# Kernel optimization log

Hardware: AMD Instinct MI355X
Metric: run time of the kernel (lower is better)

## Reference

```python
import jax, jax.numpy as jnp
import numpy as np

WS = (4, 4, 4)          # window size (d, h, w)
NUM_HEADS = 6
DIM = 192


def _relative_position_index(ws):
    # static int index, computed in numpy
    coords = np.stack(np.meshgrid(np.arange(ws[0]), np.arange(ws[1]), np.arange(ws[2]), indexing='ij'))  # (3, wd, wh, ww)
    coords = coords.reshape(3, -1)                      # (3, N)
    rel = coords[:, :, None] - coords[:, None, :]        # (3, N, N)
    rel = rel.transpose(1, 2, 0)                         # (N, N, 3)
    rel[:, :, 0] += ws[0] - 1
    rel[:, :, 1] += ws[1] - 1
    rel[:, :, 2] += ws[2] - 1
    rel[:, :, 0] *= (2 * ws[1] - 1) * (2 * ws[2] - 1)
    rel[:, :, 1] *= (2 * ws[2] - 1)
    return rel.sum(-1)                                   # (N, N)

_REL_IDX = _relative_position_index(WS)


def setup_inputs() -> dict:
    key = jax.random.key(0)
    ks = jax.random.split(key, 4)
    x = jax.random.normal(ks[0], (2, DIM, 46, 47, 48), dtype=jnp.float32)
    qkv_w = jax.random.normal(ks[1], (3 * DIM, DIM), dtype=jnp.float32) * 0.02
    qkv_b = jnp.zeros((3 * DIM,), dtype=jnp.float32)
    proj_w = jax.random.normal(ks[2], (DIM, DIM), dtype=jnp.float32) * 0.02
    proj_b = jnp.zeros((DIM,), dtype=jnp.float32)
    rpb_table = jax.random.normal(ks[3], ((2 * WS[0] - 1) * (2 * WS[1] - 1) * (2 * WS[2] - 1), NUM_HEADS), dtype=jnp.float32) * 0.02
    return {"x": x, "qkv_w": qkv_w, "qkv_b": qkv_b, "proj_w": proj_w, "proj_b": proj_b, "rpb_table": rpb_table}


def reference(x, qkv_w, qkv_b, proj_w, proj_b, rpb_table):
    B, C, D, H, W = x.shape
    wd, wh, ww = WS
    pd = (-D) % wd
    ph = (-H) % wh
    pw = (-W) % ww
    Dp, Hp, Wp = D + pd, H + ph, W + pw

    # BCDHW -> B,D,H,W,C then pad spatial dims (zero pad, same as F.pad on BCDHW)
    xc = jnp.transpose(x, (0, 2, 3, 4, 1))
    xc = jnp.pad(xc, ((0, 0), (0, pd), (0, ph), (0, pw), (0, 0)))

    # window partition -> (nW, N, C)
    Dw, Hw, Ww = Dp // wd, Hp // wh, Wp // ww
    xw = xc.reshape(B, Dw, wd, Hw, wh, Ww, ww, C)
    xw = jnp.transpose(xw, (0, 1, 3, 5, 2, 4, 6, 7)).reshape(-1, wd * wh * ww, C)
    N = wd * wh * ww

    # windowed MHA with relative position bias
    hd = C // NUM_HEADS
    qkv = xw @ qkv_w.T + qkv_b                               # (nW, N, 3C)
    qkv = qkv.reshape(-1, N, 3, NUM_HEADS, hd)
    q, k, v = (jnp.transpose(qkv[:, :, i], (0, 2, 1, 3)) for i in range(3))  # (nW, h, N, hd)
    scale = jnp.asarray(hd, x.dtype) ** -0.5
    attn = jnp.einsum('whnd,whmd->whnm', q * scale, k)       # (nW, h, N, N)
    bias = rpb_table[_REL_IDX.reshape(-1)].reshape(N, N, NUM_HEADS)
    bias = jnp.transpose(bias, (2, 0, 1))                    # (h, N, N)
    attn = jax.nn.softmax(attn + bias[None], axis=-1)
    out = jnp.einsum('whnm,whmd->whnd', attn, v)             # (nW, h, N, hd)
    out = jnp.transpose(out, (0, 2, 1, 3)).reshape(-1, N, C)
    out = out @ proj_w.T + proj_b

    # window reverse + crop, back to BCDHW
    xr = out.reshape(B, Dw, Hw, Ww, wd, wh, ww, C)
    xr = jnp.transpose(xr, (0, 1, 4, 2, 5, 3, 6, 7)).reshape(B, Dp, Hp, Wp, C)
    xr = jnp.transpose(xr, (0, 4, 1, 2, 3))[:, :, :D, :H, :W]
    return xr
```

## Files before the change

kernel.cpp:

```cpp
#include <hip/hip_runtime.h>

typedef __bf16 bf16x8 __attribute__((ext_vector_type(8)));
typedef __bf16 bf16x4 __attribute__((ext_vector_type(4)));
typedef float  f32x4  __attribute__((ext_vector_type(4)));

#define MFMA16(a, b, c) __builtin_amdgcn_mfma_f32_16x16x32_bf16((a), (b), (c), 0, 0, 0)

constexpr int Cdim = 192, NHd = 6;
constexpr int Dd = 46, Hh = 47, Wl = 48;
constexpr int HWst = Hh * Wl;
constexpr int NWIN_PER_B = 12 * 12 * 12;
constexpr int NBLK = 2 * NWIN_PER_B;
constexpr float SCALE = 0.17677669529663687f;

constexpr int WQ_ELEMS = 576 * 192;
constexpr int WP_ELEMS = 192 * 192;
constexpr size_t OFF_WQ   = 0;
constexpr size_t OFF_WP   = OFF_WQ + WQ_ELEMS;
constexpr size_t OFF_RPBT = OFF_WP + WP_ELEMS;
constexpr size_t WS_SMALL = (OFF_RPBT + 4128) * 2;

__device__ inline bf16x8 cvt8(const float* __restrict__ p) {
  f32x4 u0 = *(const f32x4*)p;
  f32x4 u1 = *(const f32x4*)(p + 4);
  bf16x8 r;
  r[0] = (__bf16)u0[0]; r[1] = (__bf16)u0[1]; r[2] = (__bf16)u0[2]; r[3] = (__bf16)u0[3];
  r[4] = (__bf16)u1[0]; r[5] = (__bf16)u1[1]; r[6] = (__bf16)u1[2]; r[7] = (__bf16)u1[3];
  return r;
}

__device__ inline bf16x8 cat8(bf16x4 a, bf16x4 b) {
  bf16x8 r;
  r[0] = a[0]; r[1] = a[1]; r[2] = a[2]; r[3] = a[3];
  r[4] = b[0]; r[5] = b[1]; r[6] = b[2]; r[7] = b[3];
  return r;
}

__global__ __launch_bounds__(256) void convert_w_kernel(
    const float* __restrict__ qkv_w, const float* __restrict__ proj_w,
    const float* __restrict__ rpb,
    __bf16* __restrict__ wq, __bf16* __restrict__ wp, float* __restrict__ rpbt) {
  const int i = blockIdx.x * 256 + threadIdx.x;
  if (i < WQ_ELEMS) wq[i] = (__bf16)qkv_w[i];
  if (i < WP_ELEMS) wp[i] = (__bf16)proj_w[i];
  if (i < 343 * NHd) {
    const int h = i / 343, idx = i % 343;
    rpbt[h * 343 + idx] = rpb[idx * NHd + h];
  }
}

constexpr int QKLD = 36;
constexpr int VLD  = 68;
constexpr int PLD  = 72;
constexpr int BUFE = 2304;

__global__ __launch_bounds__(384, 4) void fused_kernel(
    const float* __restrict__ x, const float* __restrict__ qkv_b,
    const __bf16* __restrict__ wq, const __bf16* __restrict__ wp,
    const float* __restrict__ proj_b, const float* __restrict__ rpbt,
    float* __restrict__ out)
{
  __shared__ __bf16 xw[64 * 200];
  __shared__ __bf16 bufs[6 * BUFE];
  const f32x4 fz = {0.f, 0.f, 0.f, 0.f};
  const int tid = threadIdx.x, lane = tid & 63, wv = tid >> 6;
  const int li = lane & 15, g = lane >> 4;
  const int hq = wv;
  const int bid = blockIdx.x;
  const int wid = (bid & 7) * (NBLK / 8) + (bid >> 3);
  const int b = wid / NWIN_PER_B, wr = wid % NWIN_PER_B;
  const int d0 = (wr / 144) * 4, h0 = ((wr / 12) % 12) * 4, w0 = (wr % 12) * 4;

  #pragma unroll
  for (int rep = 0; rep < 8; ++rep) {
    const int task = rep * 384 + tid;
    const int c = task % Cdim, ph = task / Cdim;
    const int dd = ph >> 2, hh = ph & 3;
    const int d = d0 + dd, hs = h0 + hh;
    f32x4 v = fz;
    if (d < Dd && hs < Hh)
      v = *(const f32x4*)(x + ((size_t)(b * Cdim + c) * Dd + d) * HWst + hs * Wl + w0);
    const int nb = (dd * 16 + hh * 4) * 200 + c;
    xw[nb]       = (__bf16)v[0];
    xw[nb + 200] = (__bf16)v[1];
    xw[nb + 400] = (__bf16)v[2];
    xw[nb + 600] = (__bf16)v[3];
  }
  __syncthreads();

  __bf16* buf = bufs + wv * BUFE;
  bf16x8 qfv[4], kfv[4], vav[2][2];

  {
    f32x4 acc[2][4];
    #pragma unroll
    for (int i = 0; i < 2; ++i)
      #pragma unroll
      for (int t = 0; t < 4; ++t) acc[i][t] = fz;
    #pragma unroll
    for (int kk = 0; kk < 6; ++kk) {
      const int k0 = kk * 32 + g * 8;
      bf16x8 xf[4];
      #pragma unroll
      for (int nt = 0; nt < 4; ++nt)
        xf[nt] = *(const bf16x8*)&xw[(nt * 16 + li) * 200 + k0];
      #pragma unroll
      for (int i = 0; i < 2; ++i) {
        bf16x8 wf = *(const bf16x8*)(wq + (size_t)((hq * 2 + i) * 16 + li) * Cdim + k0);
        #pragma unroll
        for (int nt = 0; nt < 4; ++nt)
          acc[i][nt] = MFMA16(wf, xf[nt], acc[i][nt]);
      }
    }
    #pragma unroll
    for (int i = 0; i < 2; ++i) {
      const f32x4 b4 = *(const f32x4*)(qkv_b + (hq * 2 + i) * 16 + g * 4);
      #pragma unroll
      for (int nt = 0; nt < 4; ++nt) {
        f32x4 val = (acc[i][nt] + b4) * SCALE;
        bf16x4 pk;
        pk[0] = (__bf16)val[0]; pk[1] = (__bf16)val[1];
        pk[2] = (__bf16)val[2]; pk[3] = (__bf16)val[3];
        *(bf16x4*)&buf[(nt * 16 + li) * QKLD + i * 16 + g * 4] = pk;
      }
    }
    #pragma unroll
    for (int t = 0; t < 4; ++t) {
      bf16x4 lo = *(const bf16x4*)&buf[(t * 16 + li) * QKLD + g * 8];
      bf16x4 hi = *(const bf16x4*)&buf[(t * 16 + li) * QKLD + g * 8 + 4];
      qfv[t] = cat8(lo, hi);
    }
  }

  {
    f32x4 acc[2][4];
    #pragma unroll
    for (int i = 0; i < 2; ++i)
      #pragma unroll
      for (int t = 0; t < 4; ++t) acc[i][t] = fz;
    #pragma unroll
    for (int kk = 0; kk < 6; ++kk) {
      const int k0 = kk * 32 + g * 8;
      bf16x8 xf[4];
      #pragma unroll
      for (int nt = 0; nt < 4; ++nt)
        xf[nt] = *(const bf16x8*)&xw[(nt * 16 + li) * 200 + k0];
      #pragma unroll
      for (int i = 0; i < 2; ++i) {
        bf16x8 wf = *(const bf16x8*)(wq + (size_t)(192 + (hq * 2 + i) * 16 + li) * Cdim + k0);
        #pragma unroll
        for (int nt = 0; nt < 4; ++nt)
          acc[i][nt] = MFMA16(wf, xf[nt], acc[i][nt]);
      }
    }
    #pragma unroll
    for (int i = 0; i < 2; ++i) {
      const f32x4 b4 = *(const f32x4*)(qkv_b + 192 + (hq * 2 + i) * 16 + g * 4);
      #pragma unroll
      for (int nt = 0; nt < 4; ++nt) {
        f32x4 val = acc[i][nt] + b4;
        bf16x4 pk;
        pk[0] = (__bf16)val[0]; pk[1] = (__bf16)val[1];
        pk[2] = (__bf16)val[2]; pk[3] = (__bf16)val[3];
        *(bf16x4*)&buf[(nt * 16 + li) * QKLD + i * 16 + g * 4] = pk;
      }
    }
    #pragma unroll
    for (int t = 0; t < 4; ++t) {
      bf16x4 lo = *(const bf16x4*)&buf[(t * 16 + li) * QKLD + g * 8];
      bf16x4 hi = *(const bf16x4*)&buf[(t * 16 + li) * QKLD + g * 8 + 4];
      kfv[t] = cat8(lo, hi);
    }
  }

  {
    f32x4 acc[2][4];
    #pragma unroll
    for (int i = 0; i < 2; ++i)
      #pragma unroll
      for (int t = 0; t < 4; ++t) acc[i][t] = fz;
    #pragma unroll
    for (int kk = 0; kk < 6; ++kk) {
      const int k0 = kk * 32 + g * 8;
      bf16x8 xf[4];
      #pragma unroll
      for (int rt = 0; rt < 4; ++rt)
        xf[rt] = *(const bf16x8*)&xw[(rt * 16 + li) * 200 + k0];
      #pragma unroll
      for (int i = 0; i < 2; ++i) {
        bf16x8 wf = *(const bf16x8*)(wq + (size_t)(384 + (hq * 2 + i) * 16 + li) * Cdim + k0);
        #pragma unroll
        for (int rt = 0; rt < 4; ++rt)
          acc[i][rt] = MFMA16(xf[rt], wf, acc[i][rt]);
      }
    }
    #pragma unroll
    for (int i = 0; i < 2; ++i) {
      const float bias = qkv_b[384 + (hq * 2 + i) * 16 + li];
      #pragma unroll
      for (int rt = 0; rt < 4; ++rt) {
        bf16x4 pk;
        pk[0] = (__bf16)(acc[i][rt][0] + bias);
        pk[1] = (__bf16)(acc[i][rt][1] + bias);
        pk[2] = (__bf16)(acc[i][rt][2] + bias);
        pk[3] = (__bf16)(acc[i][rt][3] + bias);
        *(bf16x4*)&buf[(i * 16 + li) * VLD + rt * 16 + g * 4] = pk;
      }
    }
    #pragma unroll
    for (int rt = 0; rt < 2; ++rt)
      #pragma unroll
      for (int kk = 0; kk < 2; ++kk) {
        bf16x4 lo = *(const bf16x4*)&buf[(rt * 16 + li) * VLD + kk * 32 + g * 8];
        bf16x4 hi = *(const bf16x4*)&buf[(rt * 16 + li) * VLD + kk * 32 + g * 8 + 4];
        vav[rt][kk] = cat8(lo, hi);
      }
  }
  __syncthreads();

  __bf16* ao = xw;

  const int hbase = ((li >> 2) - g + 3) * 7 + (li & 3) + 3;
  float brow[7][4];
  {
    const float* rp = rpbt + hq * 343 + hbase - 3;
    #pragma unroll
    for (int dd = 0; dd < 7; ++dd)
      #pragma unroll
      for (int j = 0; j < 4; ++j)
        brow[dd][j] = rp[dd * 49 + j];
  }

  __bf16* pw = buf;

  #pragma unroll
  for (int rb = 0; rb < 4; ++rb) {
    f32x4 s[4];
    #pragma unroll
    for (int ct = 0; ct < 4; ++ct) s[ct] = MFMA16(kfv[ct], qfv[rb], fz);

    float t[4][4];
    float rm = -3e38f;
    #pragma unroll
    for (int ct = 0; ct < 4; ++ct) {
      #pragma unroll
      for (int r = 0; r < 4; ++r) {
        const float tv = s[ct][r] + brow[rb - ct + 3][3 - r];
        t[ct][r] = tv;
        rm = fmaxf(rm, tv);
      }
    }
    rm = fmaxf(rm, __shfl_xor(rm, 16));
    rm = fmaxf(rm, __shfl_xor(rm, 32));
    float rs = 0.f;
    #pragma unroll
    for (int ct = 0; ct < 4; ++ct)
      #pragma unroll
      for (int r = 0; r < 4; ++r) {
        const float p = __expf(t[ct][r] - rm);
        t[ct][r] = p;
        rs += p;
      }
    rs += __shfl_xor(rs, 16);
    rs += __shfl_xor(rs, 32);
    const float rinv = 1.f / rs;

    #pragma unroll
    for (int ct = 0; ct < 4; ++ct) {
      bf16x4 pk;
      pk[0] = (__bf16)(t[ct][0] * rinv);
      pk[1] = (__bf16)(t[ct][1] * rinv);
      pk[2] = (__bf16)(t[ct][2] * rinv);
      pk[3] = (__bf16)(t[ct][3] * rinv);
      *(bf16x4*)&pw[li * PLD + ct * 16 + g * 4] = pk;
    }
    bf16x8 pa0 = *(const bf16x8*)&pw[li * PLD + g * 8];
    bf16x8 pa1 = *(const bf16x8*)&pw[li * PLD + 32 + g * 8];
    f32x4 o0 = fz, o1 = fz;
    o0 = MFMA16(vav[0][0], pa0, o0);
    o0 = MFMA16(vav[0][1], pa1, o0);
    o1 = MFMA16(vav[1][0], pa0, o1);
    o1 = MFMA16(vav[1][1], pa1, o1);
    #pragma unroll
    for (int rt = 0; rt < 2; ++rt) {
      const f32x4 o = rt ? o1 : o0;
      bf16x4 pk;
      pk[0] = (__bf16)o[0]; pk[1] = (__bf16)o[1];
      pk[2] = (__bf16)o[2]; pk[3] = (__bf16)o[3];
      *(bf16x4*)&ao[(rb * 16 + li) * 200 + hq * 32 + rt * 16 + g * 4] = pk;
    }
  }
  __syncthreads();

  f32x4 pacc[2][4];
  #pragma unroll
  for (int i = 0; i < 2; ++i)
    #pragma unroll
    for (int rt = 0; rt < 4; ++rt) pacc[i][rt] = fz;
  #pragma unroll
  for (int kk = 0; kk < 6; ++kk) {
    const int k0 = kk * 32 + g * 8;
    bf16x8 af[4];
    #pragma unroll
    for (int rt = 0; rt < 4; ++rt)
      af[rt] = *(const bf16x8*)&ao[(rt * 16 + li) * 200 + k0];
    #pragma unroll
    for (int i = 0; i < 2; ++i) {
      const int c = (wv * 2 + i) * 16 + li;
      bf16x8 bf = *(const bf16x8*)(wp + (size_t)c * Cdim + k0);
      #pragma unroll
      for (int rt = 0; rt < 4; ++rt)
        pacc[i][rt] = MFMA16(af[rt], bf, pacc[i][rt]);
    }
  }
  #pragma unroll
  for (int i = 0; i < 2; ++i) {
    const int c = (wv * 2 + i) * 16 + li;
    const float pb = proj_b[c];
    #pragma unroll
    for (int rt = 0; rt < 4; ++rt) {
      const int d = d0 + rt, hs = h0 + g;
      if (d < Dd && hs < Hh) {
        f32x4 vv = {pacc[i][rt][0] + pb, pacc[i][rt][1] + pb,
                    pacc[i][rt][2] + pb, pacc[i][rt][3] + pb};
        *(f32x4*)(out + ((size_t)(b * Cdim + c) * Dd + d) * HWst + hs * Wl + w0) = vv;
      }
    }
  }
}

constexpr int XW_LD = 200, QK_LD = 36, VT_LD = 68, P_LDF = 68;
constexpr int XW_OFF  = 0;
constexpr int Q_OFF   = 25600;
constexpr int K_OFF   = Q_OFF + 27648;
constexpr int VT_OFF  = K_OFF + 27648;
constexpr int P_OFF   = VT_OFF + 26112;
constexpr int RPB_OFF = P_OFF + 26112;
constexpr int LDS_TOTAL = RPB_OFF + 8256;

__global__ __launch_bounds__(768, 3) void winattn_fused(
    const float* __restrict__ x, const float* __restrict__ qkv_w,
    const float* __restrict__ qkv_b, const float* __restrict__ proj_w,
    const float* __restrict__ proj_b, const float* __restrict__ rpb,
    float* __restrict__ out)
{
  extern __shared__ __align__(16) char smem[];
  __bf16* xw  = (__bf16*)(smem + XW_OFF);
  __bf16* qs  = (__bf16*)(smem + Q_OFF);
  __bf16* ks  = (__bf16*)(smem + K_OFF);
  __bf16* vt  = (__bf16*)(smem + VT_OFF);
  __bf16* pl  = (__bf16*)(smem + P_OFF);
  float*  rps = (float*)(smem + RPB_OFF);
  const f32x4 fz = {0.f, 0.f, 0.f, 0.f};
  const int tid = threadIdx.x, lane = tid & 63, wv = tid >> 6;
  const int hq = wv >> 1, half = wv & 1, li = lane & 15, g = lane >> 4;
  const int bid = blockIdx.x;
  const int wid = (bid & 7) * (NBLK / 8) + (bid >> 3);
  const int b = wid / NWIN_PER_B, wr = wid % NWIN_PER_B;
  const int d0 = (wr / 144) * 4, h0 = ((wr / 12) % 12) * 4, w0 = (wr % 12) * 4;
  for (int i = tid; i < 343 * NHd; i += 768) rps[i] = rpb[i];
  #pragma unroll
  for (int rep = 0; rep < 4; ++rep) {
    const int task = rep * 768 + tid;
    const int c = task % Cdim, ph = task / Cdim;
    const int dd = ph >> 2, hh2 = ph & 3;
    const int d = d0 + dd, hsp = h0 + hh2;
    f32x4 v = fz;
    if (d < Dd && hsp < Hh)
      v = *(const f32x4*)(x + ((size_t)(b * Cdim + c) * Dd + d) * HWst + hsp * Wl + w0);
    const int nb = (dd * 16 + hh2 * 4) * XW_LD + c;
    xw[nb] = (__bf16)v[0]; xw[nb + XW_LD] = (__bf16)v[1];
    xw[nb + 2 * XW_LD] = (__bf16)v[2]; xw[nb + 3 * XW_LD] = (__bf16)v[3];
  }
  __syncthreads();
  {
    f32x4 acc[6][2];
    #pragma unroll
    for (int it = 0; it < 6; ++it)
      #pragma unroll
      for (int rr = 0; rr < 2; ++rr) acc[it][rr] = fz;
    #pragma unroll
    for (int kk = 0; kk < 6; ++kk) {
      const int k0 = kk * 32 + g * 8;
      bf16x8 af[2];
      #pragma unroll
      for (int rr = 0; rr < 2; ++rr)
        af[rr] = *(const bf16x8*)&xw[((half * 2 + rr) * 16 + li) * XW_LD + k0];
      #pragma unroll
      for (int it = 0; it < 6; ++it) {
        const int T = (it >> 1) * 12 + hq * 2 + (it & 1);
        const int j = T * 16 + li;
        bf16x8 bf = cvt8(qkv_w + j * Cdim + k0);
        #pragma unroll
        for (int rr = 0; rr < 2; ++rr) acc[it][rr] = MFMA16(af[rr], bf, acc[it][rr]);
      }
    }
    #pragma unroll
    for (int it = 0; it < 6; ++it) {
      const int part = it >> 1, e16 = (it & 1) * 16;
      const int j0 = (part * 12 + hq * 2 + (it & 1)) * 16;
      const float qb = qkv_b[j0 + li];
      #pragma unroll
      for (int rr = 0; rr < 2; ++rr) {
        const int rb = half * 2 + rr;
        #pragma unroll
        for (int r = 0; r < 4; ++r) {
          const float val = acc[it][rr][r] + qb;
          const int n = rb * 16 + g * 4 + r;
          if (part == 0)      qs[(hq * 64 + n) * QK_LD + e16 + li] = (__bf16)val;
          else if (part == 1) ks[(hq * 64 + n) * QK_LD + e16 + li] = (__bf16)val;
          else                vt[(hq * 32 + e16 + li) * VT_LD + n] = (__bf16)val;
        }
      }
    }
  }
  __syncthreads();
  {
    __bf16* pw = pl + wv * 16 * P_LDF;
    #pragma unroll 1
    for (int rr = 0; rr < 2; ++rr) {
      const int rb = half * 2 + rr;
      bf16x8 aq = *(const bf16x8*)&qs[(hq * 64 + rb * 16 + li) * QK_LD + g * 8];
      f32x4 s[4];
      #pragma unroll
      for (int ct = 0; ct < 4; ++ct) {
        bf16x8 bk = *(const bf16x8*)&ks[(hq * 64 + ct * 16 + li) * QK_LD + g * 8];
        s[ct] = MFMA16(aq, bk, fz);
      }
      float t[4][4], rm[4] = {-3e38f, -3e38f, -3e38f, -3e38f};
      #pragma unroll
      for (int ct = 0; ct < 4; ++ct) {
        #pragma unroll
        for (int r = 0; r < 4; ++r) {
          const int idx = (rb - ct + 3) * 49 + (g - (li >> 2) + 3) * 7 + (r - (li & 3) + 3);
          const float tv = s[ct][r] * SCALE + rps[idx * NHd + hq];
          t[ct][r] = tv;
          rm[r] = fmaxf(rm[r], tv);
        }
      }
      #pragma unroll
      for (int r = 0; r < 4; ++r) {
        rm[r] = fmaxf(rm[r], __shfl_xor(rm[r], 1, 16));
        rm[r] = fmaxf(rm[r], __shfl_xor(rm[r], 2, 16));
        rm[r] = fmaxf(rm[r], __shfl_xor(rm[r], 4, 16));
        rm[r] = fmaxf(rm[r], __shfl_xor(rm[r], 8, 16));
      }
      float rs[4] = {0, 0, 0, 0};
      #pragma unroll
      for (int ct = 0; ct < 4; ++ct)
        #pragma unroll
        for (int r = 0; r < 4; ++r) {
          const float p = __expf(t[ct][r] - rm[r]);
          t[ct][r] = p; rs[r] += p;
        }
      #pragma unroll
      for (int r = 0; r < 4; ++r) {
        rs[r] += __shfl_xor(rs[r], 1, 16);
        rs[r] += __shfl_xor(rs[r], 2, 16);
        rs[r] += __shfl_xor(rs[r], 4, 16);
        rs[r] += __shfl_xor(rs[r], 8, 16);
      }
      #pragma unroll
      for (int ct = 0; ct < 4; ++ct)
        #pragma unroll
        for (int r = 0; r < 4; ++r)
          pw[(g * 4 + r) * P_LDF + ct * 16 + li] = (__bf16)t[ct][r];
      f32x4 o[2] = {fz, fz};
      #pragma unroll
      for (int kk = 0; kk < 2; ++kk) {
        bf16x8 ap = *(const bf16x8*)&pw[li * P_LDF + kk * 32 + g * 8];
        #pragma unroll
        for (int ct = 0; ct < 2; ++ct) {
          bf16x8 bv = *(const bf16x8*)&vt[(hq * 32 + ct * 16 + li) * VT_LD + kk * 32 + g * 8];
          o[ct] = MFMA16(ap, bv, o[ct]);
        }
      }
      float inv[4];
      #pragma unroll
      for (int r = 0; r < 4; ++r) inv[r] = 1.f / rs[r];
      #pragma unroll
      for (int ct = 0; ct < 2; ++ct)
        #pragma unroll
        for (int r = 0; r < 4; ++r)
          xw[(rb * 16 + g * 4 + r) * XW_LD + hq * 32 + ct * 16 + li] = (__bf16)(o[ct][r] * inv[r]);
    }
  }
  __syncthreads();
  {
    f32x4 acc[4];
    #pragma unroll
    for (int rt = 0; rt < 4; ++rt) acc[rt] = fz;
    const int c = wv * 16 + li;
    #pragma unroll
    for (int kk = 0; kk < 6; ++kk) {
      const int k0 = kk * 32 + g * 8;
      bf16x8 bf = cvt8(proj_w + c * Cdim + k0);
      #pragma unroll
      for (int rt = 0; rt < 4; ++rt) {
        bf16x8 af = *(const bf16x8*)&xw[(rt * 16 + li) * XW_LD + k0];
        acc[rt] = MFMA16(af, bf, acc[rt]);
      }
    }
    const float pb = proj_b[c];
    #pragma unroll
    for (int rt = 0; rt < 4; ++rt) {
      const int d = d0 + rt, hsp = h0 + g;
      if (d < Dd && hsp < Hh) {
        f32x4 vv = {acc[rt][0] + pb, acc[rt][1] + pb, acc[rt][2] + pb, acc[rt][3] + pb};
        *(f32x4*)(out + ((size_t)(b * Cdim + c) * Dd + d) * HWst + hsp * Wl + w0) = vv;
      }
    }
  }
}

extern "C" void kernel_launch(void* const* d_in, const int* in_sizes, int n_in,
                              void* d_out, int out_size, void* d_ws, size_t ws_size,
                              hipStream_t stream) {
  const float* x      = (const float*)d_in[0];
  const float* qkv_w  = (const float*)d_in[1];
  const float* qkv_b  = (const float*)d_in[2];
  const float* proj_w = (const float*)d_in[3];
  const float* proj_b = (const float*)d_in[4];
  const float* rpb    = (const float*)d_in[5];
  float* out = (float*)d_out;

  if (ws_size >= WS_SMALL) {
    __bf16* wsb  = (__bf16*)d_ws;
    __bf16* wq   = wsb + OFF_WQ;
    __bf16* wp   = wsb + OFF_WP;
    float*  rpbt = (float*)(wsb + OFF_RPBT);
    convert_w_kernel<<<(WQ_ELEMS + 255) / 256, 256, 0, stream>>>(qkv_w, proj_w, rpb, wq, wp, rpbt);
    fused_kernel<<<NBLK, 384, 0, stream>>>(x, qkv_b, wq, wp, proj_b, rpbt, out);
  } else {
    (void)hipFuncSetAttribute(reinterpret_cast<const void*>(&winattn_fused),
                              hipFuncAttributeMaxDynamicSharedMemorySize, LDS_TOTAL);
    winattn_fused<<<NBLK, 768, LDS_TOTAL, stream>>>(
        x, qkv_w, qkv_b, proj_w, proj_b, rpb, out);
  }
}
```

Measured before the change: 292.7 us.

## Keep Q/K/V/P MFMA operands in registers instead of LDS round-trips

Drops the per-wave shared-memory staging buffers used to re-layout the Q, K, V projection outputs and the softmax probabilities into MFMA operand form. It builds them directly in registers by concatenating packed accumulator fragments, which works because a permuted contraction order is consistent across both operands. This removes LDS writes and reads and cuts shared memory per block, which may raise occupancy. It also changes the xw row stride from 200 to 204 to alter the bank-conflict pattern.

```diff
diff --git a/kernel.cpp b/kernel.cpp
--- a/kernel.cpp
+++ b/kernel.cpp
@@ -26,6 +26,12 @@
   bf16x8 r;
   r[0] = (__bf16)u0[0]; r[1] = (__bf16)u0[1]; r[2] = (__bf16)u0[2]; r[3] = (__bf16)u0[3];
   r[4] = (__bf16)u1[0]; r[5] = (__bf16)u1[1]; r[6] = (__bf16)u1[2]; r[7] = (__bf16)u1[3];
+  return r;
+}
+
+__device__ inline bf16x4 pack4(f32x4 v) {
+  bf16x4 r;
+  r[0] = (__bf16)v[0]; r[1] = (__bf16)v[1]; r[2] = (__bf16)v[2]; r[3] = (__bf16)v[3];
   return r;
 }
 
@@ -49,10 +55,7 @@
   }
 }
 
-constexpr int QKLD = 36;
-constexpr int VLD  = 68;
-constexpr int PLD  = 72;
-constexpr int BUFE = 2304;
+constexpr int XWLD = 204;
 
 __global__ __launch_bounds__(384, 4) void fused_kernel(
     const float* __restrict__ x, const float* __restrict__ qkv_b,
@@ -60,8 +63,7 @@
     const float* __restrict__ proj_b, const float* __restrict__ rpbt,
     float* __restrict__ out)
 {
-  __shared__ __bf16 xw[64 * 200];
-  __shared__ __bf16 bufs[6 * BUFE];
+  __shared__ __bf16 xw[64 * XWLD];
   const f32x4 fz = {0.f, 0.f, 0.f, 0.f};
   const int tid = threadIdx.x, lane = tid & 63, wv = tid >> 6;
   const int li = lane & 15, g = lane >> 4;
@@ -80,16 +82,15 @@
     f32x4 v = fz;
     if (d < Dd && hs < Hh)
       v = *(const f32x4*)(x + ((size_t)(b * Cdim + c) * Dd + d) * HWst + hs * Wl + w0);
-    const int nb = (dd * 16 + hh * 4) * 200 + c;
-    xw[nb]       = (__bf16)v[0];
-    xw[nb + 200] = (__bf16)v[1];
-    xw[nb + 400] = (__bf16)v[2];
-    xw[nb + 600] = (__bf16)v[3];
-  }
-  __syncthreads();
-
-  __bf16* buf = bufs + wv * BUFE;
-  bf16x8 qfv[4], kfv[4], vav[2][2];
+    const int nb = (dd * 16 + hh * 4) * XWLD + c;
+    xw[nb]            = (__bf16)v[0];
+    xw[nb + XWLD]     = (__bf16)v[1];
+    xw[nb + 2 * XWLD] = (__bf16)v[2];
+    xw[nb + 3 * XWLD] = (__bf16)v[3];
+  }
+  __syncthreads();
+
+  bf16x8 qcat[4], kcat[4], vcat[2][2];
 
   {
     f32x4 acc[2][4];
@@ -103,7 +104,7 @@
       bf16x8 xf[4];
       #pragma unroll
       for (int nt = 0; nt < 4; ++nt)
-        xf[nt] = *(const bf16x8*)&xw[(nt * 16 + li) * 200 + k0];
+        xf[nt] = *(const bf16x8*)&xw[(nt * 16 + li) * XWLD + k0];
       #pragma unroll
       for (int i = 0; i < 2; ++i) {
         bf16x8 wf = *(const bf16x8*)(wq + (size_t)((hq * 2 + i) * 16 + li) * Cdim + k0);
@@ -112,24 +113,12 @@
           acc[i][nt] = MFMA16(wf, xf[nt], acc[i][nt]);
       }
     }
-    #pragma unroll
-    for (int i = 0; i < 2; ++i) {
-      const f32x4 b4 = *(const f32x4*)(qkv_b + (hq * 2 + i) * 16 + g * 4);
-      #pragma unroll
-      for (int nt = 0; nt < 4; ++nt) {
-        f32x4 val = (acc[i][nt] + b4) * SCALE;
-        bf16x4 pk;
-        pk[0] = (__bf16)val[0]; pk[1] = (__bf16)val[1];
-        pk[2] = (__bf16)val[2]; pk[3] = (__bf16)val[3];
-        *(bf16x4*)&buf[(nt * 16 + li) * QKLD + i * 16 + g * 4] = pk;
-      }
-    }
-    #pragma unroll
-    for (int t = 0; t < 4; ++t) {
-      bf16x4 lo = *(const bf16x4*)&buf[(t * 16 + li) * QKLD + g * 8];
-      bf16x4 hi = *(const bf16x4*)&buf[(t * 16 + li) * QKLD + g * 8 + 4];
-      qfv[t] = cat8(lo, hi);
-    }
+    const f32x4 b0 = *(const f32x4*)(qkv_b + (hq * 2) * 16 + g * 4);
+    const f32x4 b1 = *(const f32x4*)(qkv_b + (hq * 2 + 1) * 16 + g * 4);
+    #pragma unroll
+    for (int nt = 0; nt < 4; ++nt)
+      qcat[nt] = cat8(pack4((acc[0][nt] + b0) * SCALE),
+                      pack4((acc[1][nt] + b1) * SCALE));
   }
 
   {
@@ -144,7 +133,7 @@
       bf16x8 xf[4];
       #pragma unroll
       for (int nt = 0; nt < 4; ++nt)
-        xf[nt] = *(const bf16x8*)&xw[(nt * 16 + li) * 200 + k0];
+        xf[nt] = *(const bf16x8*)&xw[(nt * 16 + li) * XWLD + k0];
       #pragma unroll
       for (int i = 0; i < 2; ++i) {
         bf16x8 wf = *(const bf16x8*)(wq + (size_t)(192 + (hq * 2 + i) * 16 + li) * Cdim + k0);
@@ -153,24 +142,11 @@
           acc[i][nt] = MFMA16(wf, xf[nt], acc[i][nt]);
       }
     }
-    #pragma unroll
-    for (int i = 0; i < 2; ++i) {
-      const f32x4 b4 = *(const f32x4*)(qkv_b + 192 + (hq * 2 + i) * 16 + g * 4);
-      #pragma unroll
-      for (int nt = 0; nt < 4; ++nt) {
-        f32x4 val = acc[i][nt] + b4;
-        bf16x4 pk;
-        pk[0] = (__bf16)val[0]; pk[1] = (__bf16)val[1];
-        pk[2] = (__bf16)val[2]; pk[3] = (__bf16)val[3];
-        *(bf16x4*)&buf[(nt * 16 + li) * QKLD + i * 16 + g * 4] = pk;
-      }
-    }
-    #pragma unroll
-    for (int t = 0; t < 4; ++t) {
-      bf16x4 lo = *(const bf16x4*)&buf[(t * 16 + li) * QKLD + g * 8];
-      bf16x4 hi = *(const bf16x4*)&buf[(t * 16 + li) * QKLD + g * 8 + 4];
-      kfv[t] = cat8(lo, hi);
-    }
+    const f32x4 b0 = *(const f32x4*)(qkv_b + 192 + (hq * 2) * 16 + g * 4);
+    const f32x4 b1 = *(const f32x4*)(qkv_b + 192 + (hq * 2 + 1) * 16 + g * 4);
+    #pragma unroll
+    for (int nt = 0; nt < 4; ++nt)
+      kcat[nt] = cat8(pack4(acc[0][nt] + b0), pack4(acc[1][nt] + b1));
   }
 
   {
@@ -185,7 +161,7 @@
       bf16x8 xf[4];
       #pragma unroll
       for (int rt = 0; rt < 4; ++rt)
-        xf[rt] = *(const bf16x8*)&xw[(rt * 16 + li) * 200 + k0];
+        xf[rt] = *(const bf16x8*)&xw[(rt * 16 + li) * XWLD + k0];
       #pragma unroll
       for (int i = 0; i < 2; ++i) {
         bf16x8 wf = *(const bf16x8*)(wq + (size_t)(384 + (hq * 2 + i) * 16 + li) * Cdim + k0);
@@ -194,27 +170,16 @@
           acc[i][rt] = MFMA16(xf[rt], wf, acc[i][rt]);
       }
     }
+    const float bias0 = qkv_b[384 + (hq * 2) * 16 + li];
+    const float bias1 = qkv_b[384 + (hq * 2 + 1) * 16 + li];
+    const f32x4 vb0 = {bias0, bias0, bias0, bias0};
+    const f32x4 vb1 = {bias1, bias1, bias1, bias1};
     #pragma unroll
     for (int i = 0; i < 2; ++i) {
-      const float bias = qkv_b[384 + (hq * 2 + i) * 16 + li];
-      #pragma unroll
-      for (int rt = 0; rt < 4; ++rt) {
-        bf16x4 pk;
-        pk[0] = (__bf16)(acc[i][rt][0] + bias);
-        pk[1] = (__bf16)(acc[i][rt][1] + bias);
-        pk[2] = (__bf16)(acc[i][rt][2] + bias);
-        pk[3] = (__bf16)(acc[i][rt][3] + bias);
-        *(bf16x4*)&buf[(i * 16 + li) * VLD + rt * 16 + g * 4] = pk;
-      }
-    }
-    #pragma unroll
-    for (int rt = 0; rt < 2; ++rt)
-      #pragma unroll
-      for (int kk = 0; kk < 2; ++kk) {
-        bf16x4 lo = *(const bf16x4*)&buf[(rt * 16 + li) * VLD + kk * 32 + g * 8];
-        bf16x4 hi = *(const bf16x4*)&buf[(rt * 16 + li) * VLD + kk * 32 + g * 8 + 4];
-        vav[rt][kk] = cat8(lo, hi);
-      }
+      const f32x4 vb = i ? vb1 : vb0;
+      vcat[i][0] = cat8(pack4(acc[i][0] + vb), pack4(acc[i][1] + vb));
+      vcat[i][1] = cat8(pack4(acc[i][2] + vb), pack4(acc[i][3] + vb));
+    }
   }
   __syncthreads();
 
@@ -231,13 +196,11 @@
         brow[dd][j] = rp[dd * 49 + j];
   }
 
-  __bf16* pw = buf;
-
   #pragma unroll
   for (int rb = 0; rb < 4; ++rb) {
     f32x4 s[4];
     #pragma unroll
-    for (int ct = 0; ct < 4; ++ct) s[ct] = MFMA16(kfv[ct], qfv[rb], fz);
+    for (int ct = 0; ct < 4; ++ct) s[ct] = MFMA16(kcat[ct], qcat[rb], fz);
 
     float t[4][4];
     float rm = -3e38f;
@@ -265,29 +228,24 @@
     rs += __shfl_xor(rs, 32);
     const float rinv = 1.f / rs;
 
+    bf16x4 ppk[4];
     #pragma unroll
     for (int ct = 0; ct < 4; ++ct) {
-      bf16x4 pk;
-      pk[0] = (__bf16)(t[ct][0] * rinv);
-      pk[1] = (__bf16)(t[ct][1] * rinv);
-      pk[2] = (__bf16)(t[ct][2] * rinv);
-      pk[3] = (__bf16)(t[ct][3] * rinv);
-      *(bf16x4*)&pw[li * PLD + ct * 16 + g * 4] = pk;
-    }
-    bf16x8 pa0 = *(const bf16x8*)&pw[li * PLD + g * 8];
-    bf16x8 pa1 = *(const bf16x8*)&pw[li * PLD + 32 + g * 8];
+      f32x4 pv = {t[ct][0] * rinv, t[ct][1] * rinv, t[ct][2] * rinv, t[ct][3] * rinv};
+      ppk[ct] = pack4(pv);
+    }
+    bf16x8 pa0 = cat8(ppk[0], ppk[1]);
+    bf16x8 pa1 = cat8(ppk[2], ppk[3]);
+
     f32x4 o0 = fz, o1 = fz;
-    o0 = MFMA16(vav[0][0], pa0, o0);
-    o0 = MFMA16(vav[0][1], pa1, o0);
-    o1 = MFMA16(vav[1][0], pa0, o1);
-    o1 = MFMA16(vav[1][1], pa1, o1);
-    #pragma unroll
-    for (int rt = 0; rt < 2; ++rt) {
-      const f32x4 o = rt ? o1 : o0;
-      bf16x4 pk;
-      pk[0] = (__bf16)o[0]; pk[1] = (__bf16)o[1];
-      pk[2] = (__bf16)o[2]; pk[3] = (__bf16)o[3];
-      *(bf16x4*)&ao[(rb * 16 + li) * 200 + hq * 32 + rt * 16 + g * 4] = pk;
+    o0 = MFMA16(vcat[0][0], pa0, o0);
+    o0 = MFMA16(vcat[0][1], pa1, o0);
+    o1 = MFMA16(vcat[1][0], pa0, o1);
+    o1 = MFMA16(vcat[1][1], pa1, o1);
+    #pragma unroll
+    for (int i = 0; i < 2; ++i) {
+      const f32x4 o = i ? o1 : o0;
+      *(bf16x4*)&ao[(rb * 16 + li) * XWLD + hq * 32 + i * 16 + g * 4] = pack4(o);
     }
   }
   __syncthreads();
@@ -303,7 +261,7 @@
     bf16x8 af[4];
     #pragma unroll
     for (int rt = 0; rt < 4; ++rt)
-      af[rt] = *(const bf16x8*)&ao[(rt * 16 + li) * 200 + k0];
+      af[rt] = *(const bf16x8*)&ao[(rt * 16 + li) * XWLD + k0];
     #pragma unroll
     for (int i = 0; i < 2; ++i) {
       const int c = (wv * 2 + i) * 16 + li;
```

Measured after the change: 506.3 us. 1.73x slower.
